# Performance work log

Hardware: AMD Instinct MI355X
Metric: run time of the kernel (lower is better)

The kernel has to match this reference:

```python
import jax, jax.numpy as jnp
import numpy as np

B, N, D = 2, 2048, 1024
RANK, HEADS = 256, 16
HS = RANK // HEADS          # 16, low-rank head size for QK
DH = D // HEADS             # 64, value head size
SCALE = 1.0 / np.sqrt(HS)


def setup_inputs() -> dict:
    key = jax.random.key(0)
    k1, k2, k3 = jax.random.split(key, 3)
    x = jax.random.normal(k1, (B, N, D), dtype=jnp.float32)
    # causal additive mask, 0 on/below diag, -1e9 above
    mask = jnp.where(jnp.tril(jnp.ones((N, N), dtype=bool)), 0.0, -1e9).astype(jnp.float32)
    Wqk = jax.random.normal(k2, (2 * RANK, D), dtype=jnp.float32) * (1.0 / np.sqrt(D))
    Wv = jax.random.normal(k3, (D, D), dtype=jnp.float32) * (1.0 / np.sqrt(D))
    return {"x": x, "mask": mask, "Wqk": Wqk, "Wv": Wv}


def reference(x, mask, Wqk, Wv):
    b, n, d = x.shape
    qk = jnp.einsum('bnd,rd->bnr', x, Wqk)            # [b,n,2*rank]
    q, k = jnp.split(qk, 2, axis=-1)                  # [b,n,rank] each
    # L2 normalize over FULL rank dim (before head split), clamp norm >= 1e-6
    q = q / jnp.maximum(jnp.linalg.norm(q, axis=-1, keepdims=True), 1e-6)
    k = k / jnp.maximum(jnp.linalg.norm(k, axis=-1, keepdims=True), 1e-6)
    q = q.reshape(b, n, HEADS, HS).transpose(0, 2, 1, 3)   # [b,h,n,hs]
    k = k.reshape(b, n, HEADS, HS).transpose(0, 2, 1, 3)
    v = jnp.einsum('bnd,ed->bne', x, Wv).reshape(b, n, HEADS, DH).transpose(0, 2, 1, 3)  # [b,h,n,dh]
    att = jnp.einsum('bhqe,bhke->bhqk', q, k) * SCALE
    att = jnp.clip(att, -10000.0, 10000.0)
    att = att + mask[None, None, :, :]
    att = jax.nn.softmax(att, axis=-1)
    # NaN guard: zero NaNs then renormalize (no-op when no NaNs)
    att = jnp.where(jnp.isnan(att), 0.0, att)
    att = att / jnp.maximum(att.sum(axis=-1, keepdims=True), 1e-6)
    y = jnp.einsum('bhqk,bhkd->bhqd', att, v)              # [b,h,n,dh]
    return y.transpose(0, 2, 1, 3).reshape(b, n, d)
```

## Files before the change

kernel.cpp:

```cpp
#include <hip/hip_runtime.h>
#include <math.h>

#define BATCH 2
#define SEQ   2048
#define DIM   1024
#define RANK  256
#define HEADS 16
#define HS    16
#define DH    64
#define MROWS 4096

#define QSCALE 0.36067376f

typedef __attribute__((ext_vector_type(8)))  short    short8;
typedef __attribute__((ext_vector_type(4)))  float    f32x4;
typedef __attribute__((ext_vector_type(16))) float    f32x16;
typedef __attribute__((ext_vector_type(2)))  unsigned uint2v;

__device__ __forceinline__ unsigned short f2bf(float f) {
    union { float f; unsigned u; } v; v.f = f;
    return (unsigned short)((v.u + 0x7FFFu + ((v.u >> 16) & 1u)) >> 16);
}
__device__ __forceinline__ float bf2f(unsigned short h) {
    union { unsigned u; float f; } v; v.u = ((unsigned)h) << 16;
    return v.f;
}

#define XQ   1048576
#define WQKQ 131072
#define WVQ  262144
__global__ __launch_bounds__(256) void conv3(const float* __restrict__ x,
                                             const float* __restrict__ wqk,
                                             const float* __restrict__ wv,
                                             unsigned short* __restrict__ xb,
                                             unsigned short* __restrict__ wcat)
{
    const int i = blockIdx.x * 256 + threadIdx.x;
    const float* src; unsigned short* dst; int j;
    if (i < XQ)              { src = x;   dst = xb;   j = i; }
    else if (i < XQ + WQKQ)  { src = wqk; dst = wcat; j = i - XQ; }
    else                     { src = wv;  dst = wcat + (size_t)4 * WQKQ; j = i - XQ - WQKQ; }
    float4 v = ((const float4*)src)[j];
    ushort4 o; o.x = f2bf(v.x); o.y = f2bf(v.y); o.z = f2bf(v.z); o.w = f2bf(v.w);
    ((ushort4*)dst)[j] = o;
}

__global__ __launch_bounds__(256) void gemm_mfma(const unsigned short* __restrict__ A,
                                                 const unsigned short* __restrict__ W,
                                                 unsigned short* __restrict__ qkb,
                                                 unsigned short* __restrict__ vt)
{
    __shared__ __align__(16) unsigned short Alds[128 * 32];
    __shared__ __align__(16) unsigned short Blds[64 * 32];

    const int tid = threadIdx.x;
    const int w = tid >> 6, lane = tid & 63;
    const int lr = lane & 15, lg = lane >> 4;
    const int wm = w >> 1, wn = w & 1;
    const int bm = blockIdx.x * 128, bn = blockIdx.y * 64;

    const int srow = lane >> 2;
    const int sk   = (lane & 3) * 8;

    f32x4 acc[4][2] = {};

    for (int k0 = 0; k0 < 1024; k0 += 32) {
        __syncthreads();
        #pragma unroll
        for (int q = 0; q < 2; ++q) {
            const int r = (w * 2 + q) * 16 + srow;
            __builtin_amdgcn_global_load_lds(
                (const __attribute__((address_space(1))) unsigned int*)&A[(size_t)(bm + r) * 1024 + k0 + sk],
                (__attribute__((address_space(3))) unsigned int*)&Alds[(w * 2 + q) * 512],
                16, 0, 0);
        }
        __builtin_amdgcn_global_load_lds(
            (const __attribute__((address_space(1))) unsigned int*)&W[(size_t)(bn + w * 16 + srow) * 1024 + k0 + sk],
            (__attribute__((address_space(3))) unsigned int*)&Blds[w * 512],
            16, 0, 0);
        __syncthreads();

        short8 af[4], bfr[2];
        #pragma unroll
        for (int mi = 0; mi < 4; ++mi)
            af[mi] = *(const short8*)&Alds[(wm * 64 + mi * 16 + lr) * 32 + lg * 8];
        #pragma unroll
        for (int ni = 0; ni < 2; ++ni)
            bfr[ni] = *(const short8*)&Blds[(wn * 32 + ni * 16 + lr) * 32 + lg * 8];
        #pragma unroll
        for (int mi = 0; mi < 4; ++mi)
            #pragma unroll
            for (int ni = 0; ni < 2; ++ni)
                acc[mi][ni] = __builtin_amdgcn_mfma_f32_16x16x32_bf16(af[mi], bfr[ni], acc[mi][ni], 0, 0, 0);
    }

    if (bn < 512) {
        #pragma unroll
        for (int mi = 0; mi < 4; ++mi) {
            const int rbase = bm + wm * 64 + mi * 16 + lg * 4;
            #pragma unroll
            for (int ni = 0; ni < 2; ++ni) {
                const int col = bn + wn * 32 + ni * 16 + lr;
                #pragma unroll
                for (int r = 0; r < 4; ++r)
                    qkb[(size_t)(rbase + r) * 512 + col] = f2bf(acc[mi][ni][r]);
            }
        }
    } else {
        const int nb = bn - 512;
        #pragma unroll
        for (int mi = 0; mi < 4; ++mi) {
            const int m = bm + wm * 64 + mi * 16 + lg * 4;
            const int bb = m >> 11, ms = m & 2047;
            #pragma unroll
            for (int ni = 0; ni < 2; ++ni) {
                const int d = nb + wn * 32 + ni * 16 + lr;
                ushort4 pk;
                pk.x = f2bf(acc[mi][ni][0]); pk.y = f2bf(acc[mi][ni][1]);
                pk.z = f2bf(acc[mi][ni][2]); pk.w = f2bf(acc[mi][ni][3]);
                *(ushort4*)&vt[((size_t)bb * DIM + d) * SEQ + ms] = pk;
            }
        }
    }
}

__global__ __launch_bounds__(256) void l2norm_split(const unsigned short* __restrict__ qkb,
                                                    unsigned short* __restrict__ qn,
                                                    unsigned short* __restrict__ kn)
{
    const int row = blockIdx.x;
    const int t = threadIdx.x;
    const unsigned short* p = qkb + (size_t)row * 512;
    float q = bf2f(p[t]);
    float k = bf2f(p[t + 256]);
    float sq = q * q, sk = k * k;
    #pragma unroll
    for (int off = 32; off > 0; off >>= 1) {
        sq += __shfl_down(sq, off);
        sk += __shfl_down(sk, off);
    }
    __shared__ float sh[8];
    const int wid = t >> 6;
    if ((t & 63) == 0) { sh[wid * 2] = sq; sh[wid * 2 + 1] = sk; }
    __syncthreads();
    sq = sh[0] + sh[2] + sh[4] + sh[6];
    sk = sh[1] + sh[3] + sh[5] + sh[7];
    const float rq = QSCALE / fmaxf(sqrtf(sq), 1e-6f);
    const float rk = 1.0f   / fmaxf(sqrtf(sk), 1e-6f);
    qn[(size_t)row * 256 + t] = f2bf(q * rq);
    kn[(size_t)row * 256 + t] = f2bf(k * rk);
}


template<bool MASK>
__device__ __forceinline__ void tile32(const unsigned short* Vs, int keybase, int kh,
                                       int l31, int hi, int qg,
                                       const short8 ak0, const short8 ak1, const short8 bq,
                                       f32x16 o[2], float& lpart)
{
    const f32x16 z = {};
    const f32x16 s0 = __builtin_amdgcn_mfma_f32_32x32x16_bf16(ak0, bq, z, 0, 0, 0);
    const f32x16 s1 = __builtin_amdgcn_mfma_f32_32x32x16_bf16(ak1, bq, z, 0, 0, 0);

    float p0[16], p1[16];
    #pragma unroll
    for (int r = 0; r < 16; ++r) {
        float e0 = __builtin_exp2f(s0[r]);
        float e1 = __builtin_exp2f(s1[r]);
        if (MASK) {
            const int kl = keybase + (r & 3) + 8 * (r >> 2) + 4 * hi;
            e0 = (kl > qg) ? 0.0f : e0;
            e1 = (kl + 32 > qg) ? 0.0f : e1;
        }
        p0[r] = e0; p1[r] = e1;
        lpart += e0 + e1;
    }

    short8 pa[4];
    #pragma unroll
    for (int g = 0; g < 4; ++g) {
        const float* pc = (g < 2) ? p0 : p1;
        const int jj = 2 * (g & 1);
        unsigned a0, a1, b0, b1;
        asm("v_cvt_pk_bf16_f32 %0, %1, %2" : "=v"(a0) : "v"(pc[4*jj]),     "v"(pc[4*jj + 1]));
        asm("v_cvt_pk_bf16_f32 %0, %1, %2" : "=v"(b0) : "v"(pc[4*jj + 2]), "v"(pc[4*jj + 3]));
        asm("v_cvt_pk_bf16_f32 %0, %1, %2" : "=v"(a1) : "v"(pc[4*jj + 4]), "v"(pc[4*jj + 5]));
        asm("v_cvt_pk_bf16_f32 %0, %1, %2" : "=v"(b1) : "v"(pc[4*jj + 6]), "v"(pc[4*jj + 7]));
        const uint2v r0 = __builtin_amdgcn_permlane32_swap(a0, a1, false, false);
        const uint2v r1 = __builtin_amdgcn_permlane32_swap(b0, b1, false, false);
        union { short8 s; unsigned u[4]; } pu;
        pu.u[0] = r0[0]; pu.u[1] = r1[0]; pu.u[2] = r0[1]; pu.u[3] = r1[1];
        pa[g] = pu.s;
    }

    #pragma unroll
    for (int g = 0; g < 4; ++g)
        #pragma unroll
        for (int half = 0; half < 2; ++half) {
            const int row = half * 32 + l31;
            const short8 bv = *(const short8*)&Vs[row * 128 + ((64 * kh + 16 * g + 8 * hi) ^ (8 * (row & 7)))];
            o[half] = __builtin_amdgcn_mfma_f32_32x32x16_bf16(pa[g], bv, o[half], 0, 0, 0);
        }
}

__global__ __launch_bounds__(256, 2) void attn64(const unsigned short* __restrict__ qn,
                                                 const unsigned short* __restrict__ kn,
                                                 const unsigned short* __restrict__ vt,
                                                 float* __restrict__ out)
{
    const int L = blockIdx.x;
    const int bh = L & 31;
    const int p  = L >> 5;
    const int h = bh & 15, b = bh >> 4;

    const int tid = threadIdx.x, w = tid >> 6, lane = tid & 63;
    const int qh = w >> 1, kh = w & 1;
    const int l31 = lane & 31, hi = lane >> 5;

    __shared__ __align__(16) unsigned char smem[32768];

    const int vsub  = lane >> 4;
    const int vslot = lane & 15;

#define STAGEV(kt_, buf_) do {                                                                    \
        const int k0_ = (kt_) * 128;                                                              \
        _Pragma("unroll")                                                                         \
        for (int i = 0; i < 4; ++i) {                                                             \
            const int dh = w * 16 + i * 4 + vsub;                                                 \
            const int so = 8 * (vslot ^ (dh & 7));                                                \
            __builtin_amdgcn_global_load_lds(                                                     \
                (const __attribute__((address_space(1))) unsigned int*)                           \
                    &vt[((size_t)b * DIM + h * DH + dh) * SEQ + k0_ + so],                        \
                (__attribute__((address_space(3))) unsigned int*)(smem + (buf_) * 16384 + (w * 4 + i) * 1024), \
                16, 0, 0);                                                                        \
        }                                                                                         \
    } while (0)

    #pragma unroll 1
    for (int seg = 0; seg < 2; ++seg) {
        const int qt = seg ? p : 31 - p;
        const int qband = qt * 64 + qh * 32;
        const int qg = qband + l31;

        const short8 bq = *(const short8*)&qn[((size_t)b * SEQ + qg) * RANK + h * HS + 8 * hi];

        f32x16 o[2] = {};
        float lpart = 0.0f;

        const unsigned short* kbase = kn + ((size_t)b * SEQ + 64 * kh + l31) * RANK + h * HS + 8 * hi;
        short8 ak0 = *(const short8*)kbase;
        short8 ak1 = *(const short8*)(kbase + 32 * RANK);

        const int ntiles = (qt >> 1) + 1;

        __syncthreads();
        STAGEV(0, 0);
        __syncthreads();

        for (int kt = 0; kt < ntiles - 1; ++kt) {
            STAGEV(kt + 1, (kt + 1) & 1);
            short8 an0 = *(const short8*)(kbase + (size_t)(kt + 1) * 128 * RANK);
            short8 an1 = *(const short8*)(kbase + (size_t)(kt + 1) * 128 * RANK + 32 * RANK);
            __builtin_amdgcn_s_setprio(1);
            tile32<false>((const unsigned short*)(smem + (kt & 1) * 16384),
                          kt * 128 + 64 * kh, kh, l31, hi, qg, ak0, ak1, bq, o, lpart);
            __builtin_amdgcn_s_setprio(0);
            ak0 = an0; ak1 = an1;
            __syncthreads();
        }
        {
            const int kt = ntiles - 1;
            const int wfirst = 128 * kt + 64 * kh;
            const unsigned short* Vs = (const unsigned short*)(smem + (kt & 1) * 16384);
            __builtin_amdgcn_s_setprio(1);
            if (wfirst <= qband + 31) {
                if (wfirst + 63 <= qband)
                    tile32<false>(Vs, wfirst, kh, l31, hi, qg, ak0, ak1, bq, o, lpart);
                else
                    tile32<true>(Vs, wfirst, kh, l31, hi, qg, ak0, ak1, bq, o, lpart);
            }
            __builtin_amdgcn_s_setprio(0);
        }
        __syncthreads();

        float* Osm = (float*)smem;
        float* Lsm = (float*)(smem + 16384);
        if (kh == 1) {
            #pragma unroll
            for (int half = 0; half < 2; ++half)
                #pragma unroll
                for (int r = 0; r < 16; ++r) {
                    const int q = (r & 3) + 8 * (r >> 2) + 4 * hi;
                    Osm[(qh * 32 + q) * 64 + half * 32 + l31] = o[half][r];
                }
            Lsm[qh * 64 + lane] = lpart;
        }
        __syncthreads();
        if (kh == 0) {
            float lt = lpart + Lsm[qh * 64 + lane];
            lt += __shfl_xor(lt, 32);
            const float inv = 1.0f / fmaxf(lt, 1e-6f);
            #pragma unroll
            for (int r = 0; r < 16; ++r) {
                const int q = (r & 3) + 8 * (r >> 2) + 4 * hi;
                const float iv = __shfl(inv, q);
                #pragma unroll
                for (int half = 0; half < 2; ++half) {
                    const float val = (o[half][r] + Osm[(qh * 32 + q) * 64 + half * 32 + l31]) * iv;
                    out[((size_t)b * SEQ + qband + q) * DIM + h * DH + half * 32 + l31] = val;
                }
            }
        }
    }
#undef STAGEV
}

extern "C" void kernel_launch(void* const* d_in, const int* in_sizes, int n_in,
                              void* d_out, int out_size, void* d_ws, size_t ws_size,
                              hipStream_t stream)
{
    const float* x   = (const float*)d_in[0];
    const float* Wqk = (const float*)d_in[2];
    const float* Wv  = (const float*)d_in[3];
    float* out = (float*)d_out;

    unsigned short* xb   = (unsigned short*)d_ws;
    unsigned short* qkb  = xb  + (size_t)MROWS * DIM;
    unsigned short* vt   = qkb + (size_t)MROWS * 512;
    unsigned short* wcat = vt  + (size_t)BATCH * DIM * SEQ;
    unsigned short* qn = xb;
    unsigned short* kn = xb + (size_t)MROWS * RANK;

    conv3<<<5632, 256, 0, stream>>>(x, Wqk, Wv, xb, wcat);
    gemm_mfma<<<dim3(32, 24), 256, 0, stream>>>(xb, wcat, qkb, vt);
    l2norm_split<<<MROWS, 256, 0, stream>>>(qkb, qn, kn);
    attn64<<<dim3(512), 256, 0, stream>>>(qn, kn, vt, out);
}
```

Baseline: 73.47 us.

## Fuse paired causal query tiles into one K/V sweep sharing staged tiles

Each block previously processed its two query tiles (31-p and p) one after the other, reloading the K and V tiles for each. Now both tiles are handled in a single pass over the key tiles, so every staged V tile and K fragment serves both query sets, roughly halving K/V traffic for the shorter segment and removing a second pipeline prologue. Output stores also become nontemporal. The cost is double the accumulator registers (two o arrays) at launch bounds 256,2, which risks spills or lower occupancy, plus slightly larger LDS.

New measurement: 73.29 us. Within noise of the previous version (-0.2%).

```diff
diff --git a/kernel.cpp b/kernel.cpp
--- a/kernel.cpp
+++ b/kernel.cpp
@@ -203,10 +203,25 @@
         }
 }
 
-__global__ __launch_bounds__(256, 2) void attn64(const unsigned short* __restrict__ qn,
-                                                 const unsigned short* __restrict__ kn,
-                                                 const unsigned short* __restrict__ vt,
-                                                 float* __restrict__ out)
+__device__ __forceinline__ void seg_tile(const unsigned short* Vs, int kb, int kh,
+                                         int l31, int hi, int qband, int qg, bool last,
+                                         const short8 ak0, const short8 ak1, const short8 bq,
+                                         f32x16 o[2], float& lpart)
+{
+    if (!last) {
+        tile32<false>(Vs, kb, kh, l31, hi, qg, ak0, ak1, bq, o, lpart);
+    } else if (kb <= qband + 31) {
+        if (kb + 63 <= qband)
+            tile32<false>(Vs, kb, kh, l31, hi, qg, ak0, ak1, bq, o, lpart);
+        else
+            tile32<true>(Vs, kb, kh, l31, hi, qg, ak0, ak1, bq, o, lpart);
+    }
+}
+
+__global__ __launch_bounds__(256, 2) void attn_pair(const unsigned short* __restrict__ qn,
+                                                    const unsigned short* __restrict__ kn,
+                                                    const unsigned short* __restrict__ vt,
+                                                    float* __restrict__ out)
 {
     const int L = blockIdx.x;
     const int bh = L & 31;
@@ -217,7 +232,23 @@
     const int qh = w >> 1, kh = w & 1;
     const int l31 = lane & 31, hi = lane >> 5;
 
-    __shared__ __align__(16) unsigned char smem[32768];
+    const int qt0 = 31 - p, qt1 = p;
+    const int nt0 = (qt0 >> 1) + 1;
+    const int nt1 = (qt1 >> 1) + 1;
+    const int qband0 = qt0 * 64 + qh * 32, qband1 = qt1 * 64 + qh * 32;
+    const int qg0 = qband0 + l31, qg1 = qband1 + l31;
+
+    __shared__ __align__(16) unsigned char smem[33792];
+
+    const short8 bq0 = *(const short8*)&qn[((size_t)b * SEQ + qg0) * RANK + h * HS + 8 * hi];
+    const short8 bq1 = *(const short8*)&qn[((size_t)b * SEQ + qg1) * RANK + h * HS + 8 * hi];
+
+    f32x16 o0[2] = {}, o1[2] = {};
+    float lp0 = 0.0f, lp1 = 0.0f;
+
+    const unsigned short* kbase = kn + ((size_t)b * SEQ + 64 * kh + l31) * RANK + h * HS + 8 * hi;
+    short8 ak0 = *(const short8*)kbase;
+    short8 ak1 = *(const short8*)(kbase + 32 * RANK);
 
     const int vsub  = lane >> 4;
     const int vslot = lane & 15;
@@ -236,83 +267,74 @@
         }                                                                                         \
     } while (0)
 
+    STAGEV(0, 0);
+    __syncthreads();
+
     #pragma unroll 1
-    for (int seg = 0; seg < 2; ++seg) {
-        const int qt = seg ? p : 31 - p;
-        const int qband = qt * 64 + qh * 32;
-        const int qg = qband + l31;
-
-        const short8 bq = *(const short8*)&qn[((size_t)b * SEQ + qg) * RANK + h * HS + 8 * hi];
-
-        f32x16 o[2] = {};
-        float lpart = 0.0f;
-
-        const unsigned short* kbase = kn + ((size_t)b * SEQ + 64 * kh + l31) * RANK + h * HS + 8 * hi;
-        short8 ak0 = *(const short8*)kbase;
-        short8 ak1 = *(const short8*)(kbase + 32 * RANK);
-
-        const int ntiles = (qt >> 1) + 1;
-
+    for (int kt = 0; kt < nt0; ++kt) {
+        const bool more = (kt + 1 < nt0);
+        if (more) STAGEV(kt + 1, (kt + 1) & 1);
+        short8 an0 = ak0, an1 = ak1;
+        if (more) {
+            an0 = *(const short8*)(kbase + (size_t)(kt + 1) * 128 * RANK);
+            an1 = *(const short8*)(kbase + (size_t)(kt + 1) * 128 * RANK + 32 * RANK);
+        }
+
+        const unsigned short* Vs = (const unsigned short*)(smem + (kt & 1) * 16384);
+        const int kb = kt * 128 + 64 * kh;
+
+        __builtin_amdgcn_s_setprio(1);
+        seg_tile(Vs, kb, kh, l31, hi, qband0, qg0, kt == nt0 - 1, ak0, ak1, bq0, o0, lp0);
+        if (kt < nt1)
+            seg_tile(Vs, kb, kh, l31, hi, qband1, qg1, kt == nt1 - 1, ak0, ak1, bq1, o1, lp1);
+        __builtin_amdgcn_s_setprio(0);
+
+        ak0 = an0; ak1 = an1;
         __syncthreads();
-        STAGEV(0, 0);
-        __syncthreads();
-
-        for (int kt = 0; kt < ntiles - 1; ++kt) {
-            STAGEV(kt + 1, (kt + 1) & 1);
-            short8 an0 = *(const short8*)(kbase + (size_t)(kt + 1) * 128 * RANK);
-            short8 an1 = *(const short8*)(kbase + (size_t)(kt + 1) * 128 * RANK + 32 * RANK);
-            __builtin_amdgcn_s_setprio(1);
-            tile32<false>((const unsigned short*)(smem + (kt & 1) * 16384),
-                          kt * 128 + 64 * kh, kh, l31, hi, qg, ak0, ak1, bq, o, lpart);
-            __builtin_amdgcn_s_setprio(0);
-            ak0 = an0; ak1 = an1;
-            __syncthreads();
-        }
-        {
-            const int kt = ntiles - 1;
-            const int wfirst = 128 * kt + 64 * kh;
-            const unsigned short* Vs = (const unsigned short*)(smem + (kt & 1) * 16384);
-            __builtin_amdgcn_s_setprio(1);
-            if (wfirst <= qband + 31) {
-                if (wfirst + 63 <= qband)
-                    tile32<false>(Vs, wfirst, kh, l31, hi, qg, ak0, ak1, bq, o, lpart);
-                else
-                    tile32<true>(Vs, wfirst, kh, l31, hi, qg, ak0, ak1, bq, o, lpart);
-            }
-            __builtin_amdgcn_s_setprio(0);
-        }
-        __syncthreads();
-
-        float* Osm = (float*)smem;
-        float* Lsm = (float*)(smem + 16384);
-        if (kh == 1) {
-            #pragma unroll
-            for (int half = 0; half < 2; ++half)
-                #pragma unroll
-                for (int r = 0; r < 16; ++r) {
-                    const int q = (r & 3) + 8 * (r >> 2) + 4 * hi;
-                    Osm[(qh * 32 + q) * 64 + half * 32 + l31] = o[half][r];
-                }
-            Lsm[qh * 64 + lane] = lpart;
-        }
-        __syncthreads();
-        if (kh == 0) {
-            float lt = lpart + Lsm[qh * 64 + lane];
-            lt += __shfl_xor(lt, 32);
-            const float inv = 1.0f / fmaxf(lt, 1e-6f);
+    }
+#undef STAGEV
+
+    float* Os0 = (float*)smem;
+    float* Os1 = (float*)(smem + 16384);
+    float* Ls0 = (float*)(smem + 32768);
+    float* Ls1 = (float*)(smem + 33280);
+
+    if (kh == 1) {
+        #pragma unroll
+        for (int half = 0; half < 2; ++half)
             #pragma unroll
             for (int r = 0; r < 16; ++r) {
                 const int q = (r & 3) + 8 * (r >> 2) + 4 * hi;
-                const float iv = __shfl(inv, q);
-                #pragma unroll
-                for (int half = 0; half < 2; ++half) {
-                    const float val = (o[half][r] + Osm[(qh * 32 + q) * 64 + half * 32 + l31]) * iv;
-                    out[((size_t)b * SEQ + qband + q) * DIM + h * DH + half * 32 + l31] = val;
-                }
+                Os0[(qh * 32 + q) * 64 + half * 32 + l31] = o0[half][r];
+                Os1[(qh * 32 + q) * 64 + half * 32 + l31] = o1[half][r];
             }
-        }
-    }
-#undef STAGEV
+        Ls0[qh * 64 + lane] = lp0;
+        Ls1[qh * 64 + lane] = lp1;
+    }
+    __syncthreads();
+    if (kh == 0) {
+        float lt0 = lp0 + Ls0[qh * 64 + lane];
+        float lt1 = lp1 + Ls1[qh * 64 + lane];
+        lt0 += __shfl_xor(lt0, 32);
+        lt1 += __shfl_xor(lt1, 32);
+        const float inv0 = 1.0f / fmaxf(lt0, 1e-6f);
+        const float inv1 = 1.0f / fmaxf(lt1, 1e-6f);
+        #pragma unroll
+        for (int r = 0; r < 16; ++r) {
+            const int q = (r & 3) + 8 * (r >> 2) + 4 * hi;
+            const float iv0 = __shfl(inv0, q);
+            const float iv1 = __shfl(inv1, q);
+            #pragma unroll
+            for (int half = 0; half < 2; ++half) {
+                const float v0 = (o0[half][r] + Os0[(qh * 32 + q) * 64 + half * 32 + l31]) * iv0;
+                const float v1 = (o1[half][r] + Os1[(qh * 32 + q) * 64 + half * 32 + l31]) * iv1;
+                __builtin_nontemporal_store(v0,
+                    &out[((size_t)b * SEQ + qband0 + q) * DIM + h * DH + half * 32 + l31]);
+                __builtin_nontemporal_store(v1,
+                    &out[((size_t)b * SEQ + qband1 + q) * DIM + h * DH + half * 32 + l31]);
+            }
+        }
+    }
 }
 
 extern "C" void kernel_launch(void* const* d_in, const int* in_sizes, int n_in,
@@ -334,5 +356,5 @@
     conv3<<<5632, 256, 0, stream>>>(x, Wqk, Wv, xb, wcat);
     gemm_mfma<<<dim3(32, 24), 256, 0, stream>>>(xb, wcat, qkb, vt);
     l2norm_split<<<MROWS, 256, 0, stream>>>(qkb, qn, kn);
-    attn64<<<dim3(512), 256, 0, stream>>>(qn, kn, vt, out);
-}
+    attn_pair<<<dim3(512), 256, 0, stream>>>(qn, kn, vt, out);
+}
```
